# Kernel optimization log

Hardware: AMD Instinct MI355X
Metric: run time of the kernel (lower is better)

Reference implementation:

```python
import jax, jax.numpy as jnp
import numpy as np

N_NODES = 50000


def gcn_conv(x, W, b, src, dst, n):
    # dense transform first (as PyG GCNConv does), then sparse aggregate
    h = x @ W  # [N, out]
    # add self loops
    loop = jnp.arange(n, dtype=src.dtype)
    s = jnp.concatenate([src, loop])
    d = jnp.concatenate([dst, loop])
    # symmetric normalization: deg over targets with unit edge weights
    deg = jax.ops.segment_sum(jnp.ones_like(d, dtype=h.dtype), d, num_segments=n)
    dinv = jnp.where(deg > 0, jax.lax.rsqrt(deg), 0.0)
    norm = dinv[s] * dinv[d]  # [E+N]
    msg = h[s] * norm[:, None]  # gather + scale
    out = jax.ops.segment_sum(msg, d, num_segments=n)  # scatter-add
    return out + b


def setup_inputs() -> dict:
    key = jax.random.key(0)
    k1, k2, k3, k4, k5 = jax.random.split(key, 5)
    in_dim, hid, out_dim = 256, 128, 16
    x = jax.random.normal(k1, (N_NODES, in_dim), dtype=jnp.float32)
    edge_index = jax.random.randint(k2, (2, 800000), 0, N_NODES, dtype=jnp.int64)
    # Glorot-style init for GCNConv weights, zero bias (PyG default)
    W1 = jax.random.normal(k3, (in_dim, hid), dtype=jnp.float32) / np.sqrt(in_dim)
    b1 = jnp.zeros((hid,), dtype=jnp.float32)
    W2 = jax.random.normal(k4, (hid, out_dim), dtype=jnp.float32) / np.sqrt(hid)
    b2 = jnp.zeros((out_dim,), dtype=jnp.float32)
    return {"x": x, "edge_index": edge_index, "W1": W1, "b1": b1, "W2": W2, "b2": b2}


def reference(x, edge_index, W1, b1, W2, b2):
    # eval-mode forward: dropout is identity
    src, dst = edge_index[0], edge_index[1]
    n = x.shape[0]
    h = gcn_conv(x, W1, b1, src, dst, n)
    h = jax.nn.relu(h)
    h = gcn_conv(h, W2, b2, src, dst, n)
    return jax.nn.log_softmax(h, axis=1)
```

## Files before the change

### kernel.cpp

```cpp
#include <hip/hip_runtime.h>
#include <hip/hip_bf16.h>

#define N_NODES 50000
#define E_EDGES 800000
#define IN_DIM  256
#define HID     128
#define OUT_DIM 16

#define NBUCK 391
#define NBLK  128
#define P2CAP 4096

using frag_ab = __attribute__((ext_vector_type(8))) short;
using frag_cd = __attribute__((ext_vector_type(4))) float;

static __device__ inline short f2bf(float f) {
    union { float f; unsigned u; } v; v.f = f;
    unsigned r = (v.u + 0x7fffu + ((v.u >> 16) & 1u)) >> 16;
    return (short)r;
}
static __device__ inline float bflo(unsigned u) {
    union { unsigned u; float f; } v; v.u = u << 16; return v.f;
}
static __device__ inline float bfhi(unsigned u) {
    union { unsigned u; float f; } v; v.u = u & 0xffff0000u; return v.f;
}
static __device__ inline unsigned packbf(float a, float b) {
    return (unsigned)(unsigned short)f2bf(a) | ((unsigned)(unsigned short)f2bf(b) << 16);
}


__global__ __launch_bounds__(256) void csr_a(const int4* __restrict__ dst4,
                                             int* __restrict__ cnt_bb) {
    __shared__ int h[NBUCK];
    int t = threadIdx.x;
    for (int i = t; i < NBUCK; i += 256) h[i] = 0;
    __syncthreads();
    for (int i = blockIdx.x * 256 + t; i < E_EDGES / 4; i += NBLK * 256) {
        int4 d = dst4[i];
        atomicAdd(&h[d.x >> 7], 1);
        atomicAdd(&h[d.y >> 7], 1);
        atomicAdd(&h[d.z >> 7], 1);
        atomicAdd(&h[d.w >> 7], 1);
    }
    __syncthreads();
    for (int i = t; i < NBUCK; i += 256) cnt_bb[i * NBLK + blockIdx.x] = h[i];
}

__global__ __launch_bounds__(NBLK) void csr_b1(int* __restrict__ cnt_bb,
                                               int* __restrict__ btot) {
    __shared__ int sm[NBLK];
    int b = blockIdx.x, t = threadIdx.x;
    int v = cnt_bb[b * NBLK + t];
    sm[t] = v;
    __syncthreads();
    for (int o = 1; o < NBLK; o <<= 1) {
        int u = (t >= o) ? sm[t - o] : 0;
        __syncthreads();
        sm[t] += u;
        __syncthreads();
    }
    cnt_bb[b * NBLK + t] = sm[t] - v;
    if (t == NBLK - 1) btot[b] = sm[t];
}

__global__ __launch_bounds__(512) void csr_b2_w1t(const int* __restrict__ btot,
                                                  int* __restrict__ bbase,
                                                  const float* __restrict__ W,
                                                  uint4* __restrict__ wtf) {
    int t = threadIdx.x;
    if (blockIdx.x < 8) {
        int j = blockIdx.x * 512 + t;
        int f = j >> 6, lane = j & 63;
        int kt = f >> 3, tt = f & 7;
        int m = lane & 15, q = lane >> 4;
        int c = tt * 16 + m;
        int k0 = kt * 32 + q * 8;
        unsigned p[4];
#pragma unroll
        for (int i = 0; i < 4; ++i)
            p[i] = packbf(W[(k0 + 2 * i) * HID + c], W[(k0 + 2 * i + 1) * HID + c]);
        uint4 v; v.x = p[0]; v.y = p[1]; v.z = p[2]; v.w = p[3];
        wtf[j] = v;
        return;
    }
    __shared__ int sm[512];
    int v = (t < NBUCK) ? btot[t] : 0;
    sm[t] = v;
    __syncthreads();
    for (int o = 1; o < 512; o <<= 1) {
        int u = (t >= o) ? sm[t - o] : 0;
        __syncthreads();
        sm[t] += u;
        __syncthreads();
    }
    if (t < NBUCK) bbase[t] = sm[t] - v;
    if (t == 511) bbase[NBUCK] = sm[511];
}

__global__ __launch_bounds__(256) void csr_c(const int4* __restrict__ src4,
                                             const int4* __restrict__ dst4,
                                             const int* __restrict__ cnt_bb,
                                             const int* __restrict__ bbase,
                                             unsigned* __restrict__ tmp) {
    __shared__ int run[NBUCK];
    int t = threadIdx.x;
    for (int i = t; i < NBUCK; i += 256)
        run[i] = bbase[i] + cnt_bb[i * NBLK + blockIdx.x];
    __syncthreads();
    for (int i = blockIdx.x * 256 + t; i < E_EDGES / 4; i += NBLK * 256) {
        int4 d = dst4[i];
        int4 s = src4[i];
        int p0 = atomicAdd(&run[d.x >> 7], 1);
        tmp[p0] = (unsigned)s.x | ((unsigned)(d.x & 127) << 17);
        int p1 = atomicAdd(&run[d.y >> 7], 1);
        tmp[p1] = (unsigned)s.y | ((unsigned)(d.y & 127) << 17);
        int p2 = atomicAdd(&run[d.z >> 7], 1);
        tmp[p2] = (unsigned)s.z | ((unsigned)(d.z & 127) << 17);
        int p3 = atomicAdd(&run[d.w >> 7], 1);
        tmp[p3] = (unsigned)s.w | ((unsigned)(d.w & 127) << 17);
    }
}

__global__ __launch_bounds__(256) void csr_p2(const unsigned* __restrict__ tmp,
                                              const int* __restrict__ bbase,
                                              int* __restrict__ rowptr,
                                              float* __restrict__ dinv,
                                              int* __restrict__ ssrc) {
    __shared__ unsigned ed[P2CAP];
    __shared__ int cnt[128];
    __shared__ int off[128];
    int b = blockIdx.x, t = threadIdx.x;
    int base = bbase[b];
    int m = bbase[b + 1] - base;
    if (m > P2CAP) m = P2CAP;
    if (t < 128) cnt[t] = 0;
    __syncthreads();
    for (int i = t; i < m; i += 256) {
        unsigned v = tmp[base + i];
        ed[i] = v;
        atomicAdd(&cnt[v >> 17], 1);
    }
    __syncthreads();
    if (t < 128) off[t] = cnt[t];
    __syncthreads();
    for (int o = 1; o < 128; o <<= 1) {
        int u = (t >= o && t < 128) ? off[t - o] : 0;
        __syncthreads();
        if (t < 128) off[t] += u;
        __syncthreads();
    }
    if (t < 128) {
        int node = b * 128 + t;
        int ex = off[t] - cnt[t];
        if (node < N_NODES) {
            rowptr[node] = base + ex;
            dinv[node] = rsqrtf((float)(cnt[t] + 1));
        }
        off[t] = ex;
    }
    if (b == NBUCK - 1 && t == 0) rowptr[N_NODES] = E_EDGES;
    __syncthreads();
    for (int i = t; i < m; i += 256) {
        unsigned v = ed[i];
        int p = atomicAdd(&off[v >> 17], 1);
        ssrc[base + p] = (int)(v & 0x1FFFF);
    }
}

__global__ __launch_bounds__(512) void gemm1_mfma(const float* __restrict__ x,
                                                  const uint4* __restrict__ wtf,
                                                  const float* __restrict__ dinv,
                                                  short* __restrict__ h) {
    __shared__ uint4 lwt[64 * 64];
    int tid = threadIdx.x;
#pragma unroll
    for (int i = 0; i < 8; ++i)
        lwt[i * 512 + tid] = wtf[i * 512 + tid];

    int wave = tid >> 6;
    int lane = tid & 63;
    int m = lane & 15;
    int q = lane >> 4;
    int row0 = blockIdx.x * 128 + wave * 16;
    int arow_idx = row0 + m;
    const float4* arow4 = (const float4*)(x + (size_t)(arow_idx < N_NODES ? arow_idx : 0) * IN_DIM);

    frag_ab a[8];
#pragma unroll
    for (int kt = 0; kt < 8; ++kt) {
        float4 f0 = arow4[kt * 8 + q * 2];
        float4 f1 = arow4[kt * 8 + q * 2 + 1];
        a[kt][0] = f2bf(f0.x); a[kt][1] = f2bf(f0.y); a[kt][2] = f2bf(f0.z); a[kt][3] = f2bf(f0.w);
        a[kt][4] = f2bf(f1.x); a[kt][5] = f2bf(f1.y); a[kt][6] = f2bf(f1.z); a[kt][7] = f2bf(f1.w);
    }

    frag_cd acc[8];
#pragma unroll
    for (int t = 0; t < 8; ++t) acc[t] = frag_cd{0.f, 0.f, 0.f, 0.f};

    __syncthreads();

#pragma unroll
    for (int kt = 0; kt < 8; ++kt) {
#pragma unroll
        for (int t = 0; t < 8; ++t) {
            frag_ab b = *(const frag_ab*)&lwt[(kt * 8 + t) * 64 + lane];
            acc[t] = __builtin_amdgcn_mfma_f32_16x16x32_bf16(a[kt], b, acc[t], 0, 0, 0);
        }
    }

    float dv[4];
#pragma unroll
    for (int r = 0; r < 4; ++r) {
        int orow = row0 + q * 4 + r;
        dv[r] = (orow < N_NODES) ? dinv[orow] : 0.f;
    }
#pragma unroll
    for (int t = 0; t < 8; ++t) {
#pragma unroll
        for (int r = 0; r < 4; ++r) {
            int orow = row0 + q * 4 + r;
            if (orow < N_NODES)
                h[(size_t)orow * HID + t * 16 + m] = f2bf(acc[t][r] * dv[r]);
        }
    }
}

__global__ __launch_bounds__(256) void agg1_fused(const short* __restrict__ h1s,
                                                  const float* __restrict__ dinv,
                                                  const float* __restrict__ b1,
                                                  const float* __restrict__ W2,
                                                  const int* __restrict__ rowptr,
                                                  const int* __restrict__ ssrc,
                                                  unsigned* __restrict__ h2s) {
    __shared__ float sw2[HID * OUT_DIM];
    __shared__ float srow[4][HID];
    int tid = threadIdx.x;
#pragma unroll
    for (int i = 0; i < 8; ++i) sw2[i * 256 + tid] = W2[i * 256 + tid];
    __syncthreads();

    int wave = tid >> 6;
    int lane = tid & 63;
    int node = __builtin_amdgcn_readfirstlane(blockIdx.x * 4 + wave);
    if (node >= N_NODES) return;
    int eo = lane >> 4;
    int g  = lane & 15;

    int lo = rowptr[node], hi = rowptr[node + 1];
    float a0 = 0.f, a1 = 0.f, a2 = 0.f, a3 = 0.f;
    float a4 = 0.f, a5 = 0.f, a6 = 0.f, a7 = 0.f;

    if (eo == 0) {
        uint4 u = *(const uint4*)(h1s + (size_t)node * HID + g * 8);
        a0 = bflo(u.x); a1 = bfhi(u.x); a2 = bflo(u.y); a3 = bfhi(u.y);
        a4 = bflo(u.z); a5 = bfhi(u.z); a6 = bflo(u.w); a7 = bfhi(u.w);
    }

    int e = lo;
    for (; e + 16 <= hi; e += 16) {
        int s0 = ssrc[e + eo];
        int s1 = ssrc[e + 4 + eo];
        int s2 = ssrc[e + 8 + eo];
        int s3 = ssrc[e + 12 + eo];
        uint4 u0 = *(const uint4*)(h1s + (size_t)s0 * HID + g * 8);
        uint4 u1 = *(const uint4*)(h1s + (size_t)s1 * HID + g * 8);
        uint4 u2 = *(const uint4*)(h1s + (size_t)s2 * HID + g * 8);
        uint4 u3 = *(const uint4*)(h1s + (size_t)s3 * HID + g * 8);
        a0 += bflo(u0.x); a1 += bfhi(u0.x); a2 += bflo(u0.y); a3 += bfhi(u0.y);
        a4 += bflo(u0.z); a5 += bfhi(u0.z); a6 += bflo(u0.w); a7 += bfhi(u0.w);
        a0 += bflo(u1.x); a1 += bfhi(u1.x); a2 += bflo(u1.y); a3 += bfhi(u1.y);
        a4 += bflo(u1.z); a5 += bfhi(u1.z); a6 += bflo(u1.w); a7 += bfhi(u1.w);
        a0 += bflo(u2.x); a1 += bfhi(u2.x); a2 += bflo(u2.y); a3 += bfhi(u2.y);
        a4 += bflo(u2.z); a5 += bfhi(u2.z); a6 += bflo(u2.w); a7 += bfhi(u2.w);
        a0 += bflo(u3.x); a1 += bfhi(u3.x); a2 += bflo(u3.y); a3 += bfhi(u3.y);
        a4 += bflo(u3.z); a5 += bfhi(u3.z); a6 += bflo(u3.w); a7 += bfhi(u3.w);
    }
    for (; e + 4 <= hi; e += 4) {
        int s = ssrc[e + eo];
        uint4 u = *(const uint4*)(h1s + (size_t)s * HID + g * 8);
        a0 += bflo(u.x); a1 += bfhi(u.x); a2 += bflo(u.y); a3 += bfhi(u.y);
        a4 += bflo(u.z); a5 += bfhi(u.z); a6 += bflo(u.w); a7 += bfhi(u.w);
    }
    if (eo < hi - e) {
        int s = ssrc[e + eo];
        uint4 u = *(const uint4*)(h1s + (size_t)s * HID + g * 8);
        a0 += bflo(u.x); a1 += bfhi(u.x); a2 += bflo(u.y); a3 += bfhi(u.y);
        a4 += bflo(u.z); a5 += bfhi(u.z); a6 += bflo(u.w); a7 += bfhi(u.w);
    }

    a0 += __shfl_xor(a0, 16); a1 += __shfl_xor(a1, 16);
    a2 += __shfl_xor(a2, 16); a3 += __shfl_xor(a3, 16);
    a4 += __shfl_xor(a4, 16); a5 += __shfl_xor(a5, 16);
    a6 += __shfl_xor(a6, 16); a7 += __shfl_xor(a7, 16);
    a0 += __shfl_xor(a0, 32); a1 += __shfl_xor(a1, 32);
    a2 += __shfl_xor(a2, 32); a3 += __shfl_xor(a3, 32);
    a4 += __shfl_xor(a4, 32); a5 += __shfl_xor(a5, 32);
    a6 += __shfl_xor(a6, 32); a7 += __shfl_xor(a7, 32);

    float dd = dinv[node];
    if (eo == 0) {
        float4 bA = *(const float4*)(b1 + g * 8);
        float4 bB = *(const float4*)(b1 + g * 8 + 4);
        float* sr = srow[wave] + g * 8;
        sr[0] = fmaxf(fmaf(dd, a0, bA.x), 0.f);
        sr[1] = fmaxf(fmaf(dd, a1, bA.y), 0.f);
        sr[2] = fmaxf(fmaf(dd, a2, bA.z), 0.f);
        sr[3] = fmaxf(fmaf(dd, a3, bA.w), 0.f);
        sr[4] = fmaxf(fmaf(dd, a4, bB.x), 0.f);
        sr[5] = fmaxf(fmaf(dd, a5, bB.y), 0.f);
        sr[6] = fmaxf(fmaf(dd, a6, bB.z), 0.f);
        sr[7] = fmaxf(fmaf(dd, a7, bB.w), 0.f);
    }
    const float* sr = srow[wave];
    float p = 0.f;
#pragma unroll 8
    for (int kk = 0; kk < 32; ++kk) {
        int k = eo + 4 * kk;
        p = fmaf(sr[k], sw2[k * OUT_DIM + g], p);
    }
    p += __shfl_xor(p, 16);
    p += __shfl_xor(p, 32);
    p *= dd;
    float pn = __shfl_xor(p, 1);
    if (eo == 0 && (g & 1) == 0)
        h2s[(size_t)node * 8 + (g >> 1)] = packbf(p, pn);
}

__global__ __launch_bounds__(256) void agg2_pull(const unsigned* __restrict__ h2s,
                                                 const float* __restrict__ dinv,
                                                 const float* __restrict__ b2,
                                                 const int* __restrict__ rowptr,
                                                 const int* __restrict__ ssrc,
                                                 float* __restrict__ out) {
    int wave = threadIdx.x >> 6;
    int lane = threadIdx.x & 63;
    int node = __builtin_amdgcn_readfirstlane(blockIdx.x * 4 + wave);
    if (node >= N_NODES) return;
    int eo = lane >> 3;
    int g  = lane & 7;

    int lo = rowptr[node], hi = rowptr[node + 1];
    float a0 = 0.f, a1 = 0.f;
    if (eo == 0) {
        unsigned u = h2s[(size_t)node * 8 + g];
        a0 = bflo(u); a1 = bfhi(u);
    }
    int e = lo;
    for (; e + 16 <= hi; e += 16) {
        int s0 = ssrc[e + eo];
        int s1 = ssrc[e + 8 + eo];
        unsigned u0 = h2s[(size_t)s0 * 8 + g];
        unsigned u1 = h2s[(size_t)s1 * 8 + g];
        a0 += bflo(u0); a1 += bfhi(u0);
        a0 += bflo(u1); a1 += bfhi(u1);
    }
    for (; e + 8 <= hi; e += 8) {
        int s = ssrc[e + eo];
        unsigned u = h2s[(size_t)s * 8 + g];
        a0 += bflo(u); a1 += bfhi(u);
    }
    if (eo < hi - e) {
        int s = ssrc[e + eo];
        unsigned u = h2s[(size_t)s * 8 + g];
        a0 += bflo(u); a1 += bfhi(u);
    }

    a0 += __shfl_xor(a0, 8);  a1 += __shfl_xor(a1, 8);
    a0 += __shfl_xor(a0, 16); a1 += __shfl_xor(a1, 16);
    a0 += __shfl_xor(a0, 32); a1 += __shfl_xor(a1, 32);

    float dd = dinv[node];
    float2 bb = *(const float2*)(b2 + 2 * g);
    float v0 = fmaf(dd, a0, bb.x);
    float v1 = fmaf(dd, a1, bb.y);

    float m = fmaxf(v0, v1);
#pragma unroll
    for (int msk = 1; msk < 8; msk <<= 1) m = fmaxf(m, __shfl_xor(m, msk));
    float s2 = __expf(v0 - m) + __expf(v1 - m);
#pragma unroll
    for (int msk = 1; msk < 8; msk <<= 1) s2 += __shfl_xor(s2, msk);
    float lse = m + __logf(s2);
    if (eo == 0) {
        float2 o; o.x = v0 - lse; o.y = v1 - lse;
        *(float2*)(out + (size_t)node * OUT_DIM + 2 * g) = o;
    }
}

extern "C" void kernel_launch(void* const* d_in, const int* in_sizes, int n_in,
                              void* d_out, int out_size, void* d_ws, size_t ws_size,
                              hipStream_t stream) {
    const float* x  = (const float*)d_in[0];
    const int*   ei = (const int*)d_in[1];
    const float* W1 = (const float*)d_in[2];
    const float* b1 = (const float*)d_in[3];
    const float* W2 = (const float*)d_in[4];
    const float* b2 = (const float*)d_in[5];
    float* out = (float*)d_out;

    const int n = N_NODES;
    const int e = E_EDGES;
    const int* srcp = ei;
    const int* dstp = ei + e;

    char* w = (char*)d_ws;
    int*      cnt_bb = (int*)w;        w += (size_t)NBUCK * NBLK * 4;
    int*      btot   = (int*)w;        w += (size_t)NBUCK * 4;
    int*      bbase  = (int*)w;        w += (size_t)(NBUCK + 1) * 4;
    int*      rowptr = (int*)w;        w += (size_t)(n + 1) * 4;
    float*    dinv   = (float*)w;      w += (size_t)n * 4;
    unsigned* tmp    = (unsigned*)w;   w += (size_t)e * 4;
    int*      ssrc   = (int*)w;        w += (size_t)e * 4;
    uint4*    wtf    = (uint4*)w;      w += (size_t)64 * 64 * 16;
    short*    h1s    = (short*)w;      w += (size_t)n * HID * 2;
    unsigned* h2s    = (unsigned*)w;   w += (size_t)n * 8 * 4;

    auto blk = [](long long total, int b) { return (int)((total + b - 1) / b); };

    csr_a<<<NBLK, 256, 0, stream>>>((const int4*)dstp, cnt_bb);
    csr_b1<<<NBUCK, NBLK, 0, stream>>>(cnt_bb, btot);
    csr_b2_w1t<<<9, 512, 0, stream>>>(btot, bbase, W1, wtf);
    csr_c<<<NBLK, 256, 0, stream>>>((const int4*)srcp, (const int4*)dstp, cnt_bb, bbase, tmp);
    csr_p2<<<NBUCK, 256, 0, stream>>>(tmp, bbase, rowptr, dinv, ssrc);

    gemm1_mfma<<<blk(n, 128), 512, 0, stream>>>(x, wtf, dinv, h1s);
    agg1_fused<<<blk(n, 4), 256, 0, stream>>>(h1s, dinv, b1, W2, rowptr, ssrc, h2s);

    agg2_pull<<<blk(n, 4), 256, 0, stream>>>(h2s, dinv, b2, rowptr, ssrc, out);
}
```

Baseline: 193.4 us.

## Split layer-1 aggregation from W2 projection and run projection on MFMA

The fused aggregation kernel used to stage W2 into LDS in every block and do a scalar fp32 dot product per node. It is split in two. The aggregation kernel now only applies bias and ReLU and writes a bf16 intermediate. A new 16x16x32 bf16 MFMA kernel then multiplies that by a pre-transposed bf16 W2, which is prepared by an extra block in the existing weight-prep kernel. This removes the per-block W2 staging and the scalar FMA loop. In exchange it adds a 128-wide bf16 intermediate round trip through memory, one more launch, and an extra bf16 rounding step on the hidden activations.

After: 190.5 us. No clear change (-1.5%).

```diff
diff --git a/kernel.cpp b/kernel.cpp
--- a/kernel.cpp
+++ b/kernel.cpp
@@ -67,7 +67,9 @@
 __global__ __launch_bounds__(512) void csr_b2_w1t(const int* __restrict__ btot,
                                                   int* __restrict__ bbase,
                                                   const float* __restrict__ W,
-                                                  uint4* __restrict__ wtf) {
+                                                  uint4* __restrict__ wtf,
+                                                  const float* __restrict__ W2,
+                                                  short* __restrict__ w2t) {
     int t = threadIdx.x;
     if (blockIdx.x < 8) {
         int j = blockIdx.x * 512 + t;
@@ -82,6 +84,13 @@
             p[i] = packbf(W[(k0 + 2 * i) * HID + c], W[(k0 + 2 * i + 1) * HID + c]);
         uint4 v; v.x = p[0]; v.y = p[1]; v.z = p[2]; v.w = p[3];
         wtf[j] = v;
+        return;
+    }
+    if (blockIdx.x == 9) {
+        int n0 = t >> 5, k0 = (t & 31) * 4;
+#pragma unroll
+        for (int i = 0; i < 4; ++i)
+            w2t[n0 * HID + k0 + i] = f2bf(W2[(k0 + i) * OUT_DIM + n0]);
         return;
     }
     __shared__ int sm[512];
@@ -227,28 +236,21 @@
     }
 }
 
-__global__ __launch_bounds__(256) void agg1_fused(const short* __restrict__ h1s,
-                                                  const float* __restrict__ dinv,
-                                                  const float* __restrict__ b1,
-                                                  const float* __restrict__ W2,
-                                                  const int* __restrict__ rowptr,
-                                                  const int* __restrict__ ssrc,
-                                                  unsigned* __restrict__ h2s) {
-    __shared__ float sw2[HID * OUT_DIM];
-    __shared__ float srow[4][HID];
-    int tid = threadIdx.x;
-#pragma unroll
-    for (int i = 0; i < 8; ++i) sw2[i * 256 + tid] = W2[i * 256 + tid];
-    __syncthreads();
-
-    int wave = tid >> 6;
-    int lane = tid & 63;
+__global__ __launch_bounds__(256) void agg1_pull(const short* __restrict__ h1s,
+                                                 const float* __restrict__ dinv,
+                                                 const float* __restrict__ b1,
+                                                 const int* __restrict__ rowptr,
+                                                 const int* __restrict__ ssrc,
+                                                 uint4* __restrict__ out1) {
+    int wave = threadIdx.x >> 6;
+    int lane = threadIdx.x & 63;
     int node = __builtin_amdgcn_readfirstlane(blockIdx.x * 4 + wave);
     if (node >= N_NODES) return;
     int eo = lane >> 4;
     int g  = lane & 15;
 
     int lo = rowptr[node], hi = rowptr[node + 1];
+    float dd = dinv[node];
     float a0 = 0.f, a1 = 0.f, a2 = 0.f, a3 = 0.f;
     float a4 = 0.f, a5 = 0.f, a6 = 0.f, a7 = 0.f;
 
@@ -299,33 +301,51 @@
     a4 += __shfl_xor(a4, 32); a5 += __shfl_xor(a5, 32);
     a6 += __shfl_xor(a6, 32); a7 += __shfl_xor(a7, 32);
 
-    float dd = dinv[node];
     if (eo == 0) {
         float4 bA = *(const float4*)(b1 + g * 8);
         float4 bB = *(const float4*)(b1 + g * 8 + 4);
-        float* sr = srow[wave] + g * 8;
-        sr[0] = fmaxf(fmaf(dd, a0, bA.x), 0.f);
-        sr[1] = fmaxf(fmaf(dd, a1, bA.y), 0.f);
-        sr[2] = fmaxf(fmaf(dd, a2, bA.z), 0.f);
-        sr[3] = fmaxf(fmaf(dd, a3, bA.w), 0.f);
-        sr[4] = fmaxf(fmaf(dd, a4, bB.x), 0.f);
-        sr[5] = fmaxf(fmaf(dd, a5, bB.y), 0.f);
-        sr[6] = fmaxf(fmaf(dd, a6, bB.z), 0.f);
-        sr[7] = fmaxf(fmaf(dd, a7, bB.w), 0.f);
-    }
-    const float* sr = srow[wave];
-    float p = 0.f;
-#pragma unroll 8
-    for (int kk = 0; kk < 32; ++kk) {
-        int k = eo + 4 * kk;
-        p = fmaf(sr[k], sw2[k * OUT_DIM + g], p);
-    }
-    p += __shfl_xor(p, 16);
-    p += __shfl_xor(p, 32);
-    p *= dd;
-    float pn = __shfl_xor(p, 1);
-    if (eo == 0 && (g & 1) == 0)
-        h2s[(size_t)node * 8 + (g >> 1)] = packbf(p, pn);
+        float o0 = fmaxf(fmaf(dd, a0, bA.x), 0.f);
+        float o1 = fmaxf(fmaf(dd, a1, bA.y), 0.f);
+        float o2 = fmaxf(fmaf(dd, a2, bA.z), 0.f);
+        float o3 = fmaxf(fmaf(dd, a3, bA.w), 0.f);
+        float o4 = fmaxf(fmaf(dd, a4, bB.x), 0.f);
+        float o5 = fmaxf(fmaf(dd, a5, bB.y), 0.f);
+        float o6 = fmaxf(fmaf(dd, a6, bB.z), 0.f);
+        float o7 = fmaxf(fmaf(dd, a7, bB.w), 0.f);
+        uint4 st;
+        st.x = packbf(o0, o1); st.y = packbf(o2, o3);
+        st.z = packbf(o4, o5); st.w = packbf(o6, o7);
+        out1[(size_t)node * 16 + g] = st;
+    }
+}
+
+__global__ __launch_bounds__(256) void gemm2_mfma(const short* __restrict__ out1,
+                                                  const short* __restrict__ w2t,
+                                                  const float* __restrict__ dinv,
+                                                  short* __restrict__ h2s) {
+    int wave = threadIdx.x >> 6;
+    int lane = threadIdx.x & 63;
+    int m = lane & 15;
+    int q = lane >> 4;
+    int row0 = blockIdx.x * 64 + wave * 16;
+    int arow = row0 + m;
+    if (arow >= N_NODES) arow = N_NODES - 1;
+    const short* ap = out1 + (size_t)arow * HID + q * 8;
+    const short* bp = w2t + m * HID + q * 8;
+
+    frag_cd acc = frag_cd{0.f, 0.f, 0.f, 0.f};
+#pragma unroll
+    for (int kt = 0; kt < 4; ++kt) {
+        frag_ab a = *(const frag_ab*)(ap + kt * 32);
+        frag_ab b = *(const frag_ab*)(bp + kt * 32);
+        acc = __builtin_amdgcn_mfma_f32_16x16x32_bf16(a, b, acc, 0, 0, 0);
+    }
+#pragma unroll
+    for (int r = 0; r < 4; ++r) {
+        int row = row0 + q * 4 + r;
+        if (row < N_NODES)
+            h2s[(size_t)row * OUT_DIM + m] = f2bf(acc[r] * dinv[row]);
+    }
 }
 
 __global__ __launch_bounds__(256) void agg2_pull(const unsigned* __restrict__ h2s,
@@ -414,19 +434,22 @@
     unsigned* tmp    = (unsigned*)w;   w += (size_t)e * 4;
     int*      ssrc   = (int*)w;        w += (size_t)e * 4;
     uint4*    wtf    = (uint4*)w;      w += (size_t)64 * 64 * 16;
+    short*    w2t    = (short*)w;      w += (size_t)OUT_DIM * HID * 2;
     short*    h1s    = (short*)w;      w += (size_t)n * HID * 2;
-    unsigned* h2s    = (unsigned*)w;   w += (size_t)n * 8 * 4;
+    short*    out1   = (short*)w;      w += (size_t)n * HID * 2;
+    short*    h2s    = (short*)w;      w += (size_t)n * OUT_DIM * 2;
 
     auto blk = [](long long total, int b) { return (int)((total + b - 1) / b); };
 
     csr_a<<<NBLK, 256, 0, stream>>>((const int4*)dstp, cnt_bb);
     csr_b1<<<NBUCK, NBLK, 0, stream>>>(cnt_bb, btot);
-    csr_b2_w1t<<<9, 512, 0, stream>>>(btot, bbase, W1, wtf);
+    csr_b2_w1t<<<10, 512, 0, stream>>>(btot, bbase, W1, wtf, W2, w2t);
     csr_c<<<NBLK, 256, 0, stream>>>((const int4*)srcp, (const int4*)dstp, cnt_bb, bbase, tmp);
     csr_p2<<<NBUCK, 256, 0, stream>>>(tmp, bbase, rowptr, dinv, ssrc);
 
     gemm1_mfma<<<blk(n, 128), 512, 0, stream>>>(x, wtf, dinv, h1s);
-    agg1_fused<<<blk(n, 4), 256, 0, stream>>>(h1s, dinv, b1, W2, rowptr, ssrc, h2s);
-
-    agg2_pull<<<blk(n, 4), 256, 0, stream>>>(h2s, dinv, b2, rowptr, ssrc, out);
-}
+    agg1_pull<<<blk(n, 4), 256, 0, stream>>>(h1s, dinv, b1, rowptr, ssrc, (uint4*)out1);
+
+    gemm2_mfma<<<blk(n, 64), 256, 0, stream>>>(out1, w2t, dinv, h2s);
+    agg2_pull<<<blk(n, 4), 256, 0, stream>>>((const unsigned*)h2s, dinv, b2, rowptr, ssrc, out);
+}
```
